# Optimization experiments

Hardware: AMD Instinct MI355X
Metric: run time of the kernel (lower is better)

## Reference

```python
import jax, jax.numpy as jnp
import numpy as np

N_GRAPHS = 1000
P = 300                 # nodes per ring graph
N = N_GRAPHS * P        # 300000 nodes
IN_DIM = 2
HID = 128
OUT_DIM = 2


def _ring_edges():
    idx = jnp.arange(N)
    g = idx // P
    pos = idx % P
    nxt = g * P + (pos + 1) % P
    src = jnp.concatenate([idx, nxt])
    dst = jnp.concatenate([nxt, idx])
    return jnp.stack([src, dst]), g


def setup_inputs() -> dict:
    key = jax.random.key(0)
    ks = jax.random.split(key, 11)
    edge_index, batch = _ring_edges()
    x = jax.random.normal(ks[0], (N, IN_DIM), jnp.float32)

    def glorot(k, fan_in, fan_out):
        lim = np.sqrt(6.0 / (fan_in + fan_out)).astype(np.float32)
        return jax.random.uniform(k, (fan_in, fan_out), jnp.float32, -lim, lim)

    return {
        "x": x,
        "edge_index": edge_index,
        "batch": batch,
        "W1": glorot(ks[1], IN_DIM, HID), "b1": jnp.zeros((HID,), jnp.float32),
        "W2": glorot(ks[2], HID, HID),    "b2": jnp.zeros((HID,), jnp.float32),
        "W3": glorot(ks[3], HID, HID),    "b3": jnp.zeros((HID,), jnp.float32),
        "fw1": glorot(ks[4], HID, HID),   "fb1": jnp.zeros((HID,), jnp.float32),
        "fw2": glorot(ks[5], HID, OUT_DIM), "fb2": jnp.zeros((OUT_DIM,), jnp.float32),
    }


def _gcn_conv(x, W, b, src, dst, norm):
    h = x @ W                              # [N, out]
    msg = h[src] * norm[:, None]           # gather + per-edge scale
    agg = jax.ops.segment_sum(msg, dst, num_segments=N)  # scatter-add
    return agg + b


def reference(x, edge_index, batch, W1, b1, W2, b2, W3, b3, fw1, fb1, fw2, fb2):
    loop = jnp.arange(N)
    src = jnp.concatenate([edge_index[0], loop])
    dst = jnp.concatenate([edge_index[1], loop])
    deg = jax.ops.segment_sum(jnp.ones_like(dst, jnp.float32), dst, num_segments=N)
    dis = jax.lax.rsqrt(deg)               # deg >= 1 due to self-loops
    norm = dis[src] * dis[dst]             # per-edge normalization

    h = jax.nn.relu(_gcn_conv(x, W1, b1, src, dst, norm))
    h = jax.nn.relu(_gcn_conv(h, W2, b2, src, dst, norm))
    h = jax.nn.relu(_gcn_conv(h, W3, b3, src, dst, norm))

    # global mean pool per graph
    sums = jax.ops.segment_sum(h, batch, num_segments=N_GRAPHS)
    cnts = jax.ops.segment_sum(jnp.ones((N,), jnp.float32), batch, num_segments=N_GRAPHS)
    pooled = sums / cnts[:, None]

    out = jax.nn.relu(pooled @ fw1 + fb1)
    out = out @ fw2 + fb2
    return out
```

## Files before the change

kernel.cpp:

```cpp
#include <hip/hip_runtime.h>
#include <stdint.h>

#define P    300
#define HID  128
#define NG   1000
#define NTL  19

typedef __attribute__((ext_vector_type(8))) short bf16x8;
typedef __attribute__((ext_vector_type(4))) short bf16x4;
typedef __attribute__((ext_vector_type(4))) float f32x4;

__device__ short g_wsw[2 * HID * HID];

__device__ __forceinline__ short f2bf(float f) {
    union { float f; uint32_t u; } v; v.f = f;
    uint32_t r = v.u + 0x7fffu + ((v.u >> 16) & 1u);
    return (short)(r >> 16);
}
__device__ __forceinline__ float bf2f(short s) {
    union { uint32_t u; float f; } v; v.u = ((uint32_t)(uint16_t)s) << 16;
    return v.f;
}

__global__ __launch_bounds__(256) void k_prep(const float* __restrict__ W2,
                                              const float* __restrict__ W3) {
    int b = blockIdx.x;
    const float* W = (b < 8) ? W2 : W3;
    short* dst = g_wsw + ((b < 8) ? 0 : HID * HID);
    int t  = (b & 7) * 256 + threadIdx.x;
    int f  = t >> 4;
    int kc = t & 15;
    bf16x8 o;
    #pragma unroll
    for (int j = 0; j < 8; ++j)
        o[j] = f2bf(W[(kc * 8 + j) * HID + f]);
    *(bf16x8*)&dst[(f * 16 + (kc ^ (f & 15))) * 8] = o;
}

template<int POOL>
__device__ __forceinline__ void gemm_pass(short* __restrict__ buf,
                                          short* __restrict__ Bs,
                                          short* __restrict__ halo,
                                          short* __restrict__ row0,
                                          const short* __restrict__ wsrc,
                                          const float* __restrict__ bias,
                                          float* __restrict__ pool,
                                          int tid) {
    const int lane = tid & 63;
    const int wv   = tid >> 6;
    const int q    = lane >> 4;
    const int lm   = lane & 15;

    bf16x8 wf[4];
    #pragma unroll
    for (int kk = 0; kk < 4; ++kk)
        wf[kk] = *(const bf16x8*)&wsrc[((wv * 16 + lm) * 16 + ((4 * kk + q) ^ lm)) * 8];
    f32x4 biav = *(const f32x4*)&bias[wv * 16 + q * 4];

    f32x4 psum = f32x4{0.f, 0.f, 0.f, 0.f};

    const int s_n    = tid >> 5;
    const int s_kc   = (tid >> 1) & 15;
    const int s_half = tid & 1;

    for (int nt = 0; nt < NTL; ++nt) {
        {
            int node = nt * 16 + s_n;
            bf16x4 o;
            if (node < P) {
                const short* psrc;
                if (s_n == 0) {
                    psrc = (nt == 0)
                         ? &buf[(299 * 16 + (s_kc ^ (299 & 15))) * 8]
                         : &halo[((nt + 1) & 1) * 128 + s_kc * 8];
                } else {
                    int pr = node - 1;
                    psrc = &buf[(pr * 16 + (s_kc ^ (pr & 15))) * 8];
                }
                const short* csrc = &buf[(node * 16 + (s_kc ^ (node & 15))) * 8];
                const short* nsrc;
                if (node == P - 1) nsrc = &row0[s_kc * 8];
                else { int nx = node + 1; nsrc = &buf[(nx * 16 + (s_kc ^ (nx & 15))) * 8]; }
                bf16x4 a = *(const bf16x4*)(psrc + s_half * 4);
                bf16x4 b = *(const bf16x4*)(csrc + s_half * 4);
                bf16x4 c = *(const bf16x4*)(nsrc + s_half * 4);
                #pragma unroll
                for (int j = 0; j < 4; ++j)
                    o[j] = f2bf((bf2f(a[j]) + bf2f(b[j]) + bf2f(c[j])) * (1.0f / 3.0f));
            } else {
                o = bf16x4{0, 0, 0, 0};
            }
            *(bf16x4*)&Bs[(s_n * 16 + (s_kc ^ s_n)) * 8 + s_half * 4] = o;

            if (nt == 0 && tid >= 448 && tid < 480) {
                int t3 = tid - 448, kc3 = t3 >> 1, h3 = t3 & 1;
                *(bf16x4*)&row0[kc3 * 8 + h3 * 4] =
                    *(const bf16x4*)&buf[kc3 * 8 + h3 * 4];
            }
            if (nt < NTL - 1 && tid >= 480) {
                int t2 = tid - 480, kc2 = t2 >> 1, h2 = t2 & 1;
                int R = nt * 16 + 15;
                *(bf16x4*)&halo[(nt & 1) * 128 + kc2 * 8 + h2 * 4] =
                    *(const bf16x4*)&buf[(R * 16 + (kc2 ^ (R & 15))) * 8 + h2 * 4];
            }
        }
        __syncthreads();

        f32x4 acc = f32x4{0.f, 0.f, 0.f, 0.f};
        #pragma unroll
        for (int kk = 0; kk < 4; ++kk) {
            bf16x8 bfr = *(const bf16x8*)&Bs[(lm * 16 + ((4 * kk + q) ^ lm)) * 8];
            acc = __builtin_amdgcn_mfma_f32_16x16x32_bf16(wf[kk], bfr, acc, 0, 0, 0);
        }
        int nodeC = nt * 16 + lm;
        if (POOL) {
            if (nodeC < P) {
                #pragma unroll
                for (int i = 0; i < 4; ++i) {
                    float v = acc[i] + biav[i];
                    psum[i] += (v > 0.f ? v : 0.f);
                }
            }
        } else {
            if (nodeC < P) {
                bf16x4 pk;
                #pragma unroll
                for (int i = 0; i < 4; ++i) {
                    float v = acc[i] + biav[i];
                    pk[i] = f2bf(v > 0.f ? v : 0.f);
                }
                int kc = wv * 2 + (q >> 1);
                *(bf16x4*)&buf[(nodeC * 16 + (kc ^ (nodeC & 15))) * 8 + (q & 1) * 4] = pk;
            }
        }
        __syncthreads();
    }

    if (POOL) {
        #pragma unroll
        for (int off = 1; off <= 8; off <<= 1)
            #pragma unroll
            for (int i = 0; i < 4; ++i)
                psum[i] += __shfl_xor(psum[i], off, 64);
        if (lm == 0) {
            #pragma unroll
            for (int i = 0; i < 4; ++i)
                pool[wv * 16 + q * 4 + i] = psum[i];
        }
    }
}

__global__ __launch_bounds__(512, 4) void k_graph(
        const float* __restrict__ x,
        const float* __restrict__ W1,  const float* __restrict__ b1,
        const float* __restrict__ b2v, const float* __restrict__ b3v,
        const float* __restrict__ fw1, const float* __restrict__ fb1,
        const float* __restrict__ fw2, const float* __restrict__ fb2,
        float* __restrict__ out) {
    __shared__ __align__(16) char smem[81664];
    short* buf  = (short*)smem;
    short* Bs   = (short*)(smem + 76800);
    short* halo = (short*)(smem + 80896);
    short* row0 = (short*)(smem + 81408);
    float* poolF = (float*)Bs;
    float* parts = poolF + 128;
    float* s1    = poolF + 640;

    const int g   = blockIdx.x;
    const int tid = threadIdx.x;

    {
        const float* xg = x + g * 600;
        int kc1 = tid & 15;
        float w1x[8], w1y[8], b1v[8];
        #pragma unroll
        for (int j = 0; j < 8; ++j) {
            w1x[j] = W1[kc1 * 8 + j];
            w1y[j] = W1[HID + kc1 * 8 + j];
            b1v[j] = b1[kc1 * 8 + j];
        }
        for (int it = 0; it < 10; ++it) {
            int task = it * 512 + tid;
            if (task < P * 16) {
                int node = task >> 4;
                int prev = (node == 0)     ? P - 1 : node - 1;
                int next = (node == P - 1) ? 0     : node + 1;
                float ax = (xg[2*prev]   + xg[2*node]   + xg[2*next])   * (1.0f/3.0f);
                float ay = (xg[2*prev+1] + xg[2*node+1] + xg[2*next+1]) * (1.0f/3.0f);
                bf16x8 o;
                #pragma unroll
                for (int j = 0; j < 8; ++j) {
                    float v = ax * w1x[j] + ay * w1y[j] + b1v[j];
                    o[j] = f2bf(v > 0.f ? v : 0.f);
                }
                *(bf16x8*)&buf[(node * 16 + (kc1 ^ (node & 15))) * 8] = o;
            }
        }
    }
    __syncthreads();

    gemm_pass<0>(buf, Bs, halo, row0, g_wsw,           b2v, poolF, tid);
    gemm_pass<1>(buf, Bs, halo, row0, g_wsw + HID*HID, b3v, poolF, tid);
    __syncthreads();

    {
        int f1 = tid & 127, kg = tid >> 7;
        float p = 0.f;
        const float* fw1c = fw1 + f1;
        #pragma unroll 8
        for (int k = kg * 32; k < kg * 32 + 32; ++k)
            p += poolF[k] * fw1c[k * 128];
        parts[kg * 128 + f1] = p;
    }
    __syncthreads();
    if (tid < 128) {
        float o1 = fb1[tid] +
            (parts[tid] + parts[128 + tid] + parts[256 + tid] + parts[384 + tid])
            * (1.0f / 300.0f);
        s1[tid] = o1 > 0.f ? o1 : 0.f;
    }
    __syncthreads();
    if (tid < 128) {
        int o = tid >> 6, ln = tid & 63;
        float v = s1[ln] * fw2[ln * 2 + o] + s1[ln + 64] * fw2[(ln + 64) * 2 + o];
        #pragma unroll
        for (int off = 1; off <= 32; off <<= 1)
            v += __shfl_xor(v, off, 64);
        if (ln == 0) out[g * 2 + o] = v + fb2[o];
    }
}

extern "C" void kernel_launch(void* const* d_in, const int* in_sizes, int n_in,
                              void* d_out, int out_size, void* d_ws, size_t ws_size,
                              hipStream_t stream) {
    const float* x   = (const float*)d_in[0];
    const float* W1  = (const float*)d_in[3];
    const float* b1  = (const float*)d_in[4];
    const float* W2  = (const float*)d_in[5];
    const float* b2  = (const float*)d_in[6];
    const float* W3  = (const float*)d_in[7];
    const float* b3  = (const float*)d_in[8];
    const float* fw1 = (const float*)d_in[9];
    const float* fb1 = (const float*)d_in[10];
    const float* fw2 = (const float*)d_in[11];
    const float* fb2 = (const float*)d_in[12];
    float* out = (float*)d_out;

    k_prep <<<dim3(16), dim3(256), 0, stream>>>(W2, W3);
    k_graph<<<dim3(NG), dim3(512), 0, stream>>>(x, W1, b1, b2, b3,
                                                fw1, fb1, fw2, fb2, out);
}
```

Before: 139.4 us.

## Reorder GCN layers to matmul first then ring-average MFMA outputs in registers

Each layer now runs the 128x128 MFMA on the un-averaged node features and applies the three-neighbour ring average afterwards, on fp32 accumulators, using cross-lane shuffles. This removes the separate averaging stage that wrote through an LDS staging tile, plus the halo and row0 buffers and one barrier per tile, and cuts one bf16 rounding step. The block shrinks to 256 threads, with each wave covering two feature tiles. The x slice for the graph is also staged in shared memory before layer 1. The wraparound edge cases for node 0 and node 299 get more complex, and in-place writes need a barrier per tile in the non-pool pass.

```diff
diff --git a/kernel.cpp b/kernel.cpp
--- a/kernel.cpp
+++ b/kernel.cpp
@@ -7,7 +7,6 @@
 #define NTL  19
 
 typedef __attribute__((ext_vector_type(8))) short bf16x8;
-typedef __attribute__((ext_vector_type(4))) short bf16x4;
 typedef __attribute__((ext_vector_type(4))) float f32x4;
 
 __device__ short g_wsw[2 * HID * HID];
@@ -16,10 +15,6 @@
     union { float f; uint32_t u; } v; v.f = f;
     uint32_t r = v.u + 0x7fffu + ((v.u >> 16) & 1u);
     return (short)(r >> 16);
-}
-__device__ __forceinline__ float bf2f(short s) {
-    union { uint32_t u; float f; } v; v.u = ((uint32_t)(uint16_t)s) << 16;
-    return v.f;
 }
 
 __global__ __launch_bounds__(256) void k_prep(const float* __restrict__ W2,
@@ -37,141 +32,148 @@
     *(bf16x8*)&dst[(f * 16 + (kc ^ (f & 15))) * 8] = o;
 }
 
+__device__ __forceinline__ void avg_epi(const float* G, float vp0, float vn3,
+                                        float b, float* o) {
+    o[0] = (vp0  + G[0] + G[1]) * (1.0f / 3.0f) + b;
+    o[1] = (G[0] + G[1] + G[2]) * (1.0f / 3.0f) + b;
+    o[2] = (G[1] + G[2] + G[3]) * (1.0f / 3.0f) + b;
+    o[3] = (G[2] + G[3] + vn3 ) * (1.0f / 3.0f) + b;
+    #pragma unroll
+    for (int i = 0; i < 4; ++i) o[i] = o[i] > 0.f ? o[i] : 0.f;
+}
+
+__device__ __forceinline__ void store4(short* __restrict__ buf, int nt16,
+                                       int q, int lm, int ftg, const float* o) {
+    int fh = ftg * 2 + (lm >> 3), fl = lm & 7;
+    #pragma unroll
+    for (int i = 0; i < 4; ++i) {
+        int node = nt16 + q * 4 + i;
+        buf[(node * 16 + (fh ^ (node & 15))) * 8 + fl] = f2bf(o[i]);
+    }
+}
+
 template<int POOL>
-__device__ __forceinline__ void gemm_pass(short* __restrict__ buf,
-                                          short* __restrict__ Bs,
-                                          short* __restrict__ halo,
-                                          short* __restrict__ row0,
-                                          const short* __restrict__ wsrc,
-                                          const float* __restrict__ bias,
-                                          float* __restrict__ pool,
-                                          int tid) {
-    const int lane = tid & 63;
-    const int wv   = tid >> 6;
-    const int q    = lane >> 4;
-    const int lm   = lane & 15;
-
-    bf16x8 wf[4];
-    #pragma unroll
-    for (int kk = 0; kk < 4; ++kk)
-        wf[kk] = *(const bf16x8*)&wsrc[((wv * 16 + lm) * 16 + ((4 * kk + q) ^ lm)) * 8];
-    f32x4 biav = *(const f32x4*)&bias[wv * 16 + q * 4];
-
-    f32x4 psum = f32x4{0.f, 0.f, 0.f, 0.f};
-
-    const int s_n    = tid >> 5;
-    const int s_kc   = (tid >> 1) & 15;
-    const int s_half = tid & 1;
-
-    for (int nt = 0; nt < NTL; ++nt) {
-        {
-            int node = nt * 16 + s_n;
-            bf16x4 o;
-            if (node < P) {
-                const short* psrc;
-                if (s_n == 0) {
-                    psrc = (nt == 0)
-                         ? &buf[(299 * 16 + (s_kc ^ (299 & 15))) * 8]
-                         : &halo[((nt + 1) & 1) * 128 + s_kc * 8];
-                } else {
-                    int pr = node - 1;
-                    psrc = &buf[(pr * 16 + (s_kc ^ (pr & 15))) * 8];
-                }
-                const short* csrc = &buf[(node * 16 + (s_kc ^ (node & 15))) * 8];
-                const short* nsrc;
-                if (node == P - 1) nsrc = &row0[s_kc * 8];
-                else { int nx = node + 1; nsrc = &buf[(nx * 16 + (s_kc ^ (nx & 15))) * 8]; }
-                bf16x4 a = *(const bf16x4*)(psrc + s_half * 4);
-                bf16x4 b = *(const bf16x4*)(csrc + s_half * 4);
-                bf16x4 c = *(const bf16x4*)(nsrc + s_half * 4);
-                #pragma unroll
-                for (int j = 0; j < 4; ++j)
-                    o[j] = f2bf((bf2f(a[j]) + bf2f(b[j]) + bf2f(c[j])) * (1.0f / 3.0f));
+__device__ __forceinline__ void run_pass(short* __restrict__ buf,
+                                         const short* __restrict__ wbase,
+                                         const float* __restrict__ bias,
+                                         float* __restrict__ pool, int tid) {
+    const int lane = tid & 63, u = tid >> 6, q = lane >> 4, lm = lane & 15;
+    const int ftg0 = u * 2;
+    bf16x8 wf[2][4];
+    #pragma unroll
+    for (int ft = 0; ft < 2; ++ft) {
+        int f = (ftg0 + ft) * 16 + lm;
+        #pragma unroll
+        for (int kk = 0; kk < 4; ++kk)
+            wf[ft][kk] = *(const bf16x8*)&wbase[(f * 16 + ((4 * kk + q) ^ lm)) * 8];
+    }
+    float biaf[2] = { bias[ftg0 * 16 + lm], bias[ftg0 * 16 + 16 + lm] };
+    const int sA = (q == 0) ? (48 + lm) : (lane - 16);
+    const int sB = (lane + 16) & 63;
+
+    f32x4 Gp[2], Gc[2], Gfirst[2];
+    float c15[2] = {0.f, 0.f}, r0G1[2] = {0.f, 0.f};
+    float psum[2] = {0.f, 0.f};
+
+    Gp[0] = f32x4{0.f,0.f,0.f,0.f}; Gp[1] = f32x4{0.f,0.f,0.f,0.f};
+    #pragma unroll
+    for (int kk = 0; kk < 4; ++kk) {
+        bf16x8 af = *(const bf16x8*)&buf[(lm * 16 + ((4 * kk + q) ^ lm)) * 8];
+        Gp[0] = __builtin_amdgcn_mfma_f32_16x16x32_bf16(af, wf[0][kk], Gp[0], 0, 0, 0);
+        Gp[1] = __builtin_amdgcn_mfma_f32_16x16x32_bf16(af, wf[1][kk], Gp[1], 0, 0, 0);
+    }
+    Gfirst[0] = Gp[0]; Gfirst[1] = Gp[1];
+
+    for (int t = 1; t < NTL; ++t) {
+        if (!POOL) __syncthreads();
+        const short* tb = buf + t * 2048;
+        Gc[0] = f32x4{0.f,0.f,0.f,0.f}; Gc[1] = f32x4{0.f,0.f,0.f,0.f};
+        #pragma unroll
+        for (int kk = 0; kk < 4; ++kk) {
+            bf16x8 af = *(const bf16x8*)&tb[(lm * 16 + ((4 * kk + q) ^ lm)) * 8];
+            Gc[0] = __builtin_amdgcn_mfma_f32_16x16x32_bf16(af, wf[0][kk], Gc[0], 0, 0, 0);
+            Gc[1] = __builtin_amdgcn_mfma_f32_16x16x32_bf16(af, wf[1][kk], Gc[1], 0, 0, 0);
+        }
+        #pragma unroll
+        for (int ft = 0; ft < 2; ++ft) {
+            float bpA = __shfl(Gp[ft][3], sA, 64);
+            float bpB = __shfl(Gp[ft][0], sB, 64);
+            float bpC = __shfl(Gc[ft][0], lm, 64);
+            if (t == 1) {
+                r0G1[ft] = bpC;
             } else {
-                o = bf16x4{0, 0, 0, 0};
+                float vp0 = (q == 0) ? c15[ft] : bpA;
+                float vn3 = (q == 3) ? bpC : bpB;
+                float o[4];
+                avg_epi((const float*)&Gp[ft], vp0, vn3, biaf[ft], o);
+                if (!POOL) store4(buf, (t - 1) * 16, q, lm, ftg0 + ft, o);
+                else psum[ft] += o[0] + o[1] + o[2] + o[3];
             }
-            *(bf16x4*)&Bs[(s_n * 16 + (s_kc ^ s_n)) * 8 + s_half * 4] = o;
-
-            if (nt == 0 && tid >= 448 && tid < 480) {
-                int t3 = tid - 448, kc3 = t3 >> 1, h3 = t3 & 1;
-                *(bf16x4*)&row0[kc3 * 8 + h3 * 4] =
-                    *(const bf16x4*)&buf[kc3 * 8 + h3 * 4];
-            }
-            if (nt < NTL - 1 && tid >= 480) {
-                int t2 = tid - 480, kc2 = t2 >> 1, h2 = t2 & 1;
-                int R = nt * 16 + 15;
-                *(bf16x4*)&halo[(nt & 1) * 128 + kc2 * 8 + h2 * 4] =
-                    *(const bf16x4*)&buf[(R * 16 + (kc2 ^ (R & 15))) * 8 + h2 * 4];
-            }
-        }
-        __syncthreads();
-
-        f32x4 acc = f32x4{0.f, 0.f, 0.f, 0.f};
-        #pragma unroll
-        for (int kk = 0; kk < 4; ++kk) {
-            bf16x8 bfr = *(const bf16x8*)&Bs[(lm * 16 + ((4 * kk + q) ^ lm)) * 8];
-            acc = __builtin_amdgcn_mfma_f32_16x16x32_bf16(wf[kk], bfr, acc, 0, 0, 0);
-        }
-        int nodeC = nt * 16 + lm;
-        if (POOL) {
-            if (nodeC < P) {
-                #pragma unroll
-                for (int i = 0; i < 4; ++i) {
-                    float v = acc[i] + biav[i];
-                    psum[i] += (v > 0.f ? v : 0.f);
-                }
-            }
-        } else {
-            if (nodeC < P) {
-                bf16x4 pk;
-                #pragma unroll
-                for (int i = 0; i < 4; ++i) {
-                    float v = acc[i] + biav[i];
-                    pk[i] = f2bf(v > 0.f ? v : 0.f);
-                }
-                int kc = wv * 2 + (q >> 1);
-                *(bf16x4*)&buf[(nodeC * 16 + (kc ^ (nodeC & 15))) * 8 + (q & 1) * 4] = pk;
-            }
-        }
-        __syncthreads();
+            c15[ft] = bpA;
+        }
+        Gp[0] = Gc[0]; Gp[1] = Gc[1];
+    }
+
+    if (!POOL) __syncthreads();
+    #pragma unroll
+    for (int ft = 0; ft < 2; ++ft) {
+        float bpA  = __shfl(Gp[ft][3], sA, 64);
+        float bpB  = __shfl(Gp[ft][0], sB, 64);
+        float g0r0 = __shfl(Gfirst[ft][0], lm, 64);
+        float vp0  = (q == 0) ? c15[ft] : bpA;
+        float vn3  = (q == 2) ? g0r0 : bpB;
+        float o[4];
+        avg_epi((const float*)&Gp[ft], vp0, vn3, biaf[ft], o);
+        if (q < 3) {
+            if (!POOL) store4(buf, 18 * 16, q, lm, ftg0 + ft, o);
+            else psum[ft] += o[0] + o[1] + o[2] + o[3];
+        }
+        float bpW  = __shfl(Gp[ft][3], 32 + lm, 64);
+        float bpA0 = __shfl(Gfirst[ft][3], sA, 64);
+        float bpB0 = __shfl(Gfirst[ft][0], sB, 64);
+        float vp00 = (q == 0) ? bpW : bpA0;
+        float vn30 = (q == 3) ? r0G1[ft] : bpB0;
+        float o0[4];
+        avg_epi((const float*)&Gfirst[ft], vp00, vn30, biaf[ft], o0);
+        if (!POOL) store4(buf, 0, q, lm, ftg0 + ft, o0);
+        else psum[ft] += o0[0] + o0[1] + o0[2] + o0[3];
     }
 
     if (POOL) {
         #pragma unroll
-        for (int off = 1; off <= 8; off <<= 1)
-            #pragma unroll
-            for (int i = 0; i < 4; ++i)
-                psum[i] += __shfl_xor(psum[i], off, 64);
-        if (lm == 0) {
-            #pragma unroll
-            for (int i = 0; i < 4; ++i)
-                pool[wv * 16 + q * 4 + i] = psum[i];
-        }
-    }
-}
-
-__global__ __launch_bounds__(512, 4) void k_graph(
+        for (int ft = 0; ft < 2; ++ft) {
+            psum[ft] += __shfl_xor(psum[ft], 16, 64);
+            psum[ft] += __shfl_xor(psum[ft], 32, 64);
+        }
+        if (q == 0) {
+            pool[ftg0 * 16 + lm]      = psum[0];
+            pool[ftg0 * 16 + 16 + lm] = psum[1];
+        }
+    }
+}
+
+__global__ __launch_bounds__(256, 2) void k_graph(
         const float* __restrict__ x,
         const float* __restrict__ W1,  const float* __restrict__ b1,
         const float* __restrict__ b2v, const float* __restrict__ b3v,
         const float* __restrict__ fw1, const float* __restrict__ fb1,
         const float* __restrict__ fw2, const float* __restrict__ fb2,
         float* __restrict__ out) {
-    __shared__ __align__(16) char smem[81664];
-    short* buf  = (short*)smem;
-    short* Bs   = (short*)(smem + 76800);
-    short* halo = (short*)(smem + 80896);
-    short* row0 = (short*)(smem + 81408);
-    float* poolF = (float*)Bs;
-    float* parts = poolF + 128;
-    float* s1    = poolF + 640;
-
-    const int g   = blockIdx.x;
-    const int tid = threadIdx.x;
+    __shared__ __align__(16) short buf[304 * HID];
+    __shared__ __align__(16) float scr[640];
+    float* xs    = scr;
+    float* pool  = scr;
+    float* parts = scr + 128;
+    float* s1    = scr + 384;
+
+    const int g = blockIdx.x, tid = threadIdx.x;
+
+    if (tid < 150) *(float4*)&xs[tid * 4] = *(const float4*)&x[g * 600 + tid * 4];
+    __syncthreads();
 
     {
-        const float* xg = x + g * 600;
-        int kc1 = tid & 15;
+        const int kc1 = tid & 15;
+        const int n0  = tid >> 4;
         float w1x[8], w1y[8], b1v[8];
         #pragma unroll
         for (int j = 0; j < 8; ++j) {
@@ -179,44 +181,45 @@
             w1y[j] = W1[HID + kc1 * 8 + j];
             b1v[j] = b1[kc1 * 8 + j];
         }
-        for (int it = 0; it < 10; ++it) {
-            int task = it * 512 + tid;
-            if (task < P * 16) {
-                int node = task >> 4;
+        #pragma unroll
+        for (int it = 0; it < NTL; ++it) {
+            int node = it * 16 + n0;
+            bf16x8 o;
+            if (node < P) {
                 int prev = (node == 0)     ? P - 1 : node - 1;
                 int next = (node == P - 1) ? 0     : node + 1;
-                float ax = (xg[2*prev]   + xg[2*node]   + xg[2*next])   * (1.0f/3.0f);
-                float ay = (xg[2*prev+1] + xg[2*node+1] + xg[2*next+1]) * (1.0f/3.0f);
-                bf16x8 o;
+                float ax = (xs[2*prev]   + xs[2*node]   + xs[2*next])   * (1.f/3.f);
+                float ay = (xs[2*prev+1] + xs[2*node+1] + xs[2*next+1]) * (1.f/3.f);
                 #pragma unroll
                 for (int j = 0; j < 8; ++j) {
                     float v = ax * w1x[j] + ay * w1y[j] + b1v[j];
                     o[j] = f2bf(v > 0.f ? v : 0.f);
                 }
-                *(bf16x8*)&buf[(node * 16 + (kc1 ^ (node & 15))) * 8] = o;
+            } else {
+                o = bf16x8{0, 0, 0, 0, 0, 0, 0, 0};
             }
-        }
-    }
-    __syncthreads();
-
-    gemm_pass<0>(buf, Bs, halo, row0, g_wsw,           b2v, poolF, tid);
-    gemm_pass<1>(buf, Bs, halo, row0, g_wsw + HID*HID, b3v, poolF, tid);
+            *(bf16x8*)&buf[(node * 16 + (kc1 ^ (node & 15))) * 8] = o;
+        }
+    }
+    __syncthreads();
+
+    run_pass<0>(buf, g_wsw,             b2v, pool, tid);
+    __syncthreads();
+    run_pass<1>(buf, g_wsw + HID * HID, b3v, pool, tid);
     __syncthreads();
 
     {
-        int f1 = tid & 127, kg = tid >> 7;
+        int f = tid & 127, half = tid >> 7;
         float p = 0.f;
-        const float* fw1c = fw1 + f1;
-        #pragma unroll 8
-        for (int k = kg * 32; k < kg * 32 + 32; ++k)
-            p += poolF[k] * fw1c[k * 128];
-        parts[kg * 128 + f1] = p;
+        const float* fw1c = fw1 + f;
+        #pragma unroll 4
+        for (int k = half * 64; k < half * 64 + 64; ++k)
+            p += pool[k] * fw1c[k * 128];
+        parts[half * 128 + f] = p;
     }
     __syncthreads();
     if (tid < 128) {
-        float o1 = fb1[tid] +
-            (parts[tid] + parts[128 + tid] + parts[256 + tid] + parts[384 + tid])
-            * (1.0f / 300.0f);
+        float o1 = fb1[tid] + (parts[tid] + parts[128 + tid]) * (1.0f / 300.0f);
         s1[tid] = o1 > 0.f ? o1 : 0.f;
     }
     __syncthreads();
@@ -247,6 +250,6 @@
     float* out = (float*)d_out;
 
     k_prep <<<dim3(16), dim3(256), 0, stream>>>(W2, W3);
-    k_graph<<<dim3(NG), dim3(512), 0, stream>>>(x, W1, b1, b2, b3,
+    k_graph<<<dim3(NG), dim3(256), 0, stream>>>(x, W1, b1, b2, b3,
                                                 fw1, fb1, fw2, fb2, out);
 }
```

After: 130.3 us. 6.5% less time.
